# Optimization experiments

Hardware: AMD Instinct MI355X
Metric: run time of the kernel (lower is better)

The kernel has to match this reference:

```python
import jax, jax.numpy as jnp
import numpy as np

F, A, N = 64, 128, 4096  # frames, arrays per frame, samples per signal

def setup_inputs() -> dict:
    key = jax.random.key(0)
    k1, k2, k3, k4, k5 = jax.random.split(key, 5)
    x = jax.random.normal(k1, (F, A, 2, N), dtype=jnp.float32)
    # Conv2d(1,1,(1,3)) weights == 3-tap 1D correlation kernel + scalar bias
    w_rssi = jax.random.normal(k2, (3,), dtype=jnp.float32) * 0.1
    b_rssi = jax.random.normal(k3, (), dtype=jnp.float32) * 0.1
    w_phase = jax.random.normal(k4, (3,), dtype=jnp.float32) * 0.1
    b_phase = jax.random.normal(k5, (), dtype=jnp.float32) * 0.1
    return {"x": x, "w_rssi": w_rssi, "b_rssi": b_rssi,
            "w_phase": w_phase, "b_phase": b_phase}

def _conv1x3(sig, w, b):
    # torch Conv2d is cross-correlation: out[i] = sum_k w[k]*sig[i+k] + b
    # sig: [..., N] -> [..., N-2]
    return w[0] * sig[..., :-2] + w[1] * sig[..., 1:-1] + w[2] * sig[..., 2:] + b

def reference(x, w_rssi, b_rssi, w_phase, b_phase):
    rss = x[:, :, 0, :]    # [F, A, N]
    phase = x[:, :, 1, :]  # [F, A, N]
    c_rss = _conv1x3(rss, w_rssi, b_rssi)      # [F, A, N-2]
    c_phase = _conv1x3(phase, w_phase, b_phase)  # [F, A, N-2]
    # original: cat((c_rss, c_phase), dim=1) per array -> (1,2,N-2);
    # cat over arrays on dim 0 -> (A,2,N-2); flatten per frame.
    merged = jnp.stack((c_rss, c_phase), axis=2)  # [F, A, 2, N-2]
    return merged.reshape(x.shape[0], -1)         # [F, A*2*(N-2)]
```

## Files before the change

### kernel.cpp

```cpp
#include <hip/hip_runtime.h>


#define N_IN 4096
#define N_OUT 4094
#define CHUNKS_PER_ROW 1024
#define ROWS 16384

__global__ __launch_bounds__(256) void RTGRFID_51539607553079_kernel(
    const float* __restrict__ x,
    const float* __restrict__ w_rssi,  const float* __restrict__ b_rssi,
    const float* __restrict__ w_phase, const float* __restrict__ b_phase,
    float* __restrict__ out)
{
    const unsigned tid = blockIdx.x * blockDim.x + threadIdx.x;
    const int row   = tid >> 10;
    const int chunk = tid & 1023;
    const int n     = chunk << 2;

    const int ch = row & 1;
    const float w0 = ch ? w_phase[0] : w_rssi[0];
    const float w1 = ch ? w_phase[1] : w_rssi[1];
    const float w2 = ch ? w_phase[2] : w_rssi[2];
    const float b  = ch ? b_phase[0] : b_rssi[0];

    const float4* in4 = (const float4*)(x + (long long)row * N_IN);
    const float4 a = in4[chunk];

    float s4 = 0.f, s5 = 0.f;
    if (chunk < CHUNKS_PER_ROW - 1) {
        const float4 nb = in4[chunk + 1];
        s4 = nb.x; s5 = nb.y;
    }

    const float o0 = fmaf(w0, a.x, fmaf(w1, a.y, fmaf(w2, a.z, b)));
    const float o1 = fmaf(w0, a.y, fmaf(w1, a.z, fmaf(w2, a.w, b)));
    const float o2 = fmaf(w0, a.z, fmaf(w1, a.w, fmaf(w2, s4, b)));
    const float o3 = fmaf(w0, a.w, fmaf(w1, s4, fmaf(w2, s5, b)));

    float2* out2 = (float2*)(out + (long long)row * N_OUT + n);
    out2[0] = make_float2(o0, o1);
    if (chunk < CHUNKS_PER_ROW - 1) {
        out2[1] = make_float2(o2, o3);
    }
}

extern "C" void kernel_launch(void* const* d_in, const int* in_sizes, int n_in,
                              void* d_out, int out_size, void* d_ws, size_t ws_size,
                              hipStream_t stream) {
    const float* x       = (const float*)d_in[0];
    const float* w_rssi  = (const float*)d_in[1];
    const float* b_rssi  = (const float*)d_in[2];
    const float* w_phase = (const float*)d_in[3];
    const float* b_phase = (const float*)d_in[4];
    float* out = (float*)d_out;

    const unsigned total_threads = ROWS * CHUNKS_PER_ROW;
    const unsigned block = 256;
    const unsigned grid = total_threads / block;

    RTGRFID_51539607553079_kernel<<<grid, block, 0, stream>>>(
        x, w_rssi, b_rssi, w_phase, b_phase, out);
}
```

Baseline: 434.0 us.

## Align output stores to float4 per row parity, one block per row

Each block now processes a full row, with each thread handling four strided float4 chunks. Even rows compute outputs starting at aligned input offsets. Odd rows shift the window by two elements so every output store is an aligned 16-byte vector instead of two 8-byte stores. This is meant to cut store transactions in a bandwidth-bound kernel, at the cost of extra overlapping halo loads and parity-dependent branching.

```diff
diff --git a/kernel.cpp b/kernel.cpp
--- a/kernel.cpp
+++ b/kernel.cpp
@@ -3,7 +3,6 @@
 
 #define N_IN 4096
 #define N_OUT 4094
-#define CHUNKS_PER_ROW 1024
 #define ROWS 16384
 
 __global__ __launch_bounds__(256) void RTGRFID_51539607553079_kernel(
@@ -12,35 +11,60 @@
     const float* __restrict__ w_phase, const float* __restrict__ b_phase,
     float* __restrict__ out)
 {
-    const unsigned tid = blockIdx.x * blockDim.x + threadIdx.x;
-    const int row   = tid >> 10;
-    const int chunk = tid & 1023;
-    const int n     = chunk << 2;
+    const int row = blockIdx.x;
+    const int t   = threadIdx.x;
+    const int ch  = row & 1;
 
-    const int ch = row & 1;
-    const float w0 = ch ? w_phase[0] : w_rssi[0];
-    const float w1 = ch ? w_phase[1] : w_rssi[1];
-    const float w2 = ch ? w_phase[2] : w_rssi[2];
+    const float* wsel = ch ? w_phase : w_rssi;
+    const float w0 = wsel[0];
+    const float w1 = wsel[1];
+    const float w2 = wsel[2];
     const float b  = ch ? b_phase[0] : b_rssi[0];
 
-    const float4* in4 = (const float4*)(x + (long long)row * N_IN);
-    const float4 a = in4[chunk];
+    const float4* in4 = (const float4*)(x + (size_t)row * N_IN);
+    const float2* in2 = (const float2*)in4;
+    float* outr = out + (size_t)row * N_OUT;
 
-    float s4 = 0.f, s5 = 0.f;
-    if (chunk < CHUNKS_PER_ROW - 1) {
-        const float4 nb = in4[chunk + 1];
-        s4 = nb.x; s5 = nb.y;
-    }
-
-    const float o0 = fmaf(w0, a.x, fmaf(w1, a.y, fmaf(w2, a.z, b)));
-    const float o1 = fmaf(w0, a.y, fmaf(w1, a.z, fmaf(w2, a.w, b)));
-    const float o2 = fmaf(w0, a.z, fmaf(w1, a.w, fmaf(w2, s4, b)));
-    const float o3 = fmaf(w0, a.w, fmaf(w1, s4, fmaf(w2, s5, b)));
-
-    float2* out2 = (float2*)(out + (long long)row * N_OUT + n);
-    out2[0] = make_float2(o0, o1);
-    if (chunk < CHUNKS_PER_ROW - 1) {
-        out2[1] = make_float2(o2, o3);
+    if (ch == 0) {
+        #pragma unroll
+        for (int k = 0; k < 4; ++k) {
+            const int c = t + (k << 8);
+            const float4 a = in4[c];
+            if (c < 1023) {
+                const float2 h = in2[2 * c + 2];
+                float4 o;
+                o.x = fmaf(w0, a.x, fmaf(w1, a.y, fmaf(w2, a.z, b)));
+                o.y = fmaf(w0, a.y, fmaf(w1, a.z, fmaf(w2, a.w, b)));
+                o.z = fmaf(w0, a.z, fmaf(w1, a.w, fmaf(w2, h.x, b)));
+                o.w = fmaf(w0, a.w, fmaf(w1, h.x, fmaf(w2, h.y, b)));
+                *(float4*)(outr + 4 * c) = o;
+            } else {
+                float2 o;
+                o.x = fmaf(w0, a.x, fmaf(w1, a.y, fmaf(w2, a.z, b)));
+                o.y = fmaf(w0, a.y, fmaf(w1, a.z, fmaf(w2, a.w, b)));
+                *(float2*)(outr + 4092) = o;
+            }
+        }
+    } else {
+        #pragma unroll
+        for (int k = 0; k < 4; ++k) {
+            const int c = t + (k << 8);
+            const float4 a = in4[c];
+            if (c > 0) {
+                const float2 p = in2[2 * c - 1];
+                float4 o;
+                o.x = fmaf(w0, p.x, fmaf(w1, p.y, fmaf(w2, a.x, b)));
+                o.y = fmaf(w0, p.y, fmaf(w1, a.x, fmaf(w2, a.y, b)));
+                o.z = fmaf(w0, a.x, fmaf(w1, a.y, fmaf(w2, a.z, b)));
+                o.w = fmaf(w0, a.y, fmaf(w1, a.z, fmaf(w2, a.w, b)));
+                *(float4*)(outr + 4 * c - 2) = o;
+            } else {
+                float2 o;
+                o.x = fmaf(w0, a.x, fmaf(w1, a.y, fmaf(w2, a.z, b)));
+                o.y = fmaf(w0, a.y, fmaf(w1, a.z, fmaf(w2, a.w, b)));
+                *(float2*)(outr) = o;
+            }
+        }
     }
 }
 
@@ -54,9 +78,8 @@
     const float* b_phase = (const float*)d_in[4];
     float* out = (float*)d_out;
 
-    const unsigned total_threads = ROWS * CHUNKS_PER_ROW;
+    const unsigned grid  = ROWS;
     const unsigned block = 256;
-    const unsigned grid = total_threads / block;
 
     RTGRFID_51539607553079_kernel<<<grid, block, 0, stream>>>(
         x, w_rssi, b_rssi, w_phase, b_phase, out);
```

Result: no change. 434.9 us (+0.2%).
